# Kernel tuning notes

Measured on AMD Instinct MI355X. Metric: run time of the kernel, lower is better.

The kernel has to match this reference:

```python
import jax, jax.numpy as jnp
import numpy as np

B = 1048576
VEC_SZ = 4
LUT_BITS = 8
K = 2 ** LUT_BITS  # 256 codewords


def setup_inputs() -> dict:
    key = jax.random.key(0)
    kx, kt = jax.random.split(key)
    X = jax.random.normal(kx, (B, VEC_SZ), dtype=jnp.float32)
    tlut = jax.random.normal(kt, (K, VEC_SZ), dtype=jnp.float32)  # codebook [K, vec_sz]
    return {"X": X, "tlut": tlut}


def reference(X, tlut):
    # torch.cdist(X, tlut) -> argmin is equivalent to argmin of squared distances:
    x_sq = jnp.sum(X * X, axis=-1, keepdims=True)            # [B, 1]
    c_sq = jnp.sum(tlut * tlut, axis=-1)                     # [K]
    cross = jnp.einsum('bd,kd->bk', X, tlut)                 # [B, K]
    dist2 = x_sq - 2.0 * cross + c_sq                        # [B, K]
    state = jnp.argmin(dist2, axis=-1).astype(jnp.int32)     # [B]
    hatX = jnp.take(tlut, state, axis=0)                     # gather reconstruction [B, vec_sz]
    return hatX, state
```

## Files before the change

kernel.cpp:

```cpp
#include <hip/hip_runtime.h>

#define K_CW 256
#define PPT 4

struct P8 { float4 a; float4 b; };

__global__ void vq_pack_kernel(const float* __restrict__ tlut, float* __restrict__ pk) {
    int k = threadIdx.x;
    float c0 = tlut[k * 4 + 0];
    float c1 = tlut[k * 4 + 1];
    float c2 = tlut[k * 4 + 2];
    float c3 = tlut[k * 4 + 3];
    float s = __fadd_rn(__fadd_rn(__fadd_rn(__fmul_rn(c0, c0), __fmul_rn(c1, c1)),
                                  __fmul_rn(c2, c2)),
                        __fmul_rn(c3, c3));
    pk[k * 8 + 0] = c0; pk[k * 8 + 1] = c1; pk[k * 8 + 2] = c2; pk[k * 8 + 3] = c3;
    pk[k * 8 + 4] = s;  pk[k * 8 + 5] = 0.f; pk[k * 8 + 6] = 0.f; pk[k * 8 + 7] = 0.f;
}

__global__ __launch_bounds__(256, 4) void vq_argmin_kernel(
    const float* __restrict__ X,
    const float* __restrict__ tlut,
    const float* __restrict__ pk,
    float* __restrict__ outX,
    float* __restrict__ outS,
    int B) {
    const int g = blockIdx.x * 256 + threadIdx.x;
    const int stride = B / PPT;

    const float4* __restrict__ X4 = reinterpret_cast<const float4*>(X);
    const float4* __restrict__ T4 = reinterpret_cast<const float4*>(tlut);
    const P8* __restrict__ PK = reinterpret_cast<const P8*>(pk);

    float x0[PPT], x1[PPT], x2[PPT], x3[PPT], xsq[PPT], bestd[PPT];
    int besti[PPT];

    #pragma unroll
    for (int i = 0; i < PPT; ++i) {
        const float4 xv = X4[g + i * stride];
        x0[i] = xv.x; x1[i] = xv.y; x2[i] = xv.z; x3[i] = xv.w;
        xsq[i] = __fadd_rn(__fadd_rn(__fadd_rn(__fmul_rn(xv.x, xv.x), __fmul_rn(xv.y, xv.y)),
                                     __fmul_rn(xv.z, xv.z)),
                           __fmul_rn(xv.w, xv.w));
        bestd[i] = __builtin_inff();
        besti[i] = 0;
    }

    #pragma unroll 16
    for (int k = 0; k < K_CW; ++k) {
        const P8 e = PK[k];
        const float4 c = e.a;
        const float cs = e.b.x;
        #pragma unroll
        for (int i = 0; i < PPT; ++i) {
            float cross = __fmul_rn(x0[i], c.x);
            cross = __fmaf_rn(x1[i], c.y, cross);
            cross = __fmaf_rn(x2[i], c.z, cross);
            cross = __fmaf_rn(x3[i], c.w, cross);
            float t2 = __fmaf_rn(-2.0f, cross, xsq[i]);
            float d = __fadd_rn(t2, cs);
            besti[i] = (d < bestd[i]) ? k : besti[i];
            bestd[i] = fminf(d, bestd[i]);
        }
    }

    #pragma unroll
    for (int i = 0; i < PPT; ++i) {
        const int p = g + i * stride;
        reinterpret_cast<float4*>(outX)[p] = T4[besti[i]];
        outS[p] = (float)besti[i];
    }
}

extern "C" void kernel_launch(void* const* d_in, const int* in_sizes, int n_in,
                              void* d_out, int out_size, void* d_ws, size_t ws_size,
                              hipStream_t stream) {
    const float* X    = (const float*)d_in[0];
    const float* tlut = (const float*)d_in[1];
    const int B = in_sizes[0] / 4;

    float* outX = (float*)d_out;
    float* outS = outX + (size_t)B * 4;

    float* pk = (float*)d_ws;

    vq_pack_kernel<<<1, 256, 0, stream>>>(tlut, pk);

    const int groups = B / PPT;
    const int grid = groups / 256;
    vq_argmin_kernel<<<grid, 256, 0, stream>>>(X, tlut, pk, outX, outS, B);
}
```

Measured before the change: 128.9 us.

## Use packed FP32 math over codeword pairs with interleaved codebook layout

The codebook is repacked so that each record holds two codewords' components interleaved as float2 pairs. The distance computation then uses v_pk_mul/v_pk_fma/v_pk_add inline asm with scalar-register operands, so each instruction evaluates two codewords at once. Points per thread drop from 4 to 2 and the launch bound rises to 8 blocks per CU. This cuts VALU instruction count in the cross-term math, but the argmin compare/select stays scalar. The inline asm constrains scheduling and depends on the uniform codebook loads landing in SGPRs.

```diff
diff --git a/kernel.cpp b/kernel.cpp
--- a/kernel.cpp
+++ b/kernel.cpp
@@ -1,9 +1,25 @@
 #include <hip/hip_runtime.h>
 
+typedef float f32x2 __attribute__((ext_vector_type(2)));
+
 #define K_CW 256
-#define PPT 4
+#define NJ (K_CW / 2)
+#define PPT 2
 
-struct P8 { float4 a; float4 b; };
+struct PK2 { f32x2 c0, c1, c2, c3, cs, pad; };
+
+__device__ __forceinline__ f32x2 pk_mul_vs(f32x2 a, f32x2 b) {
+    f32x2 d; asm("v_pk_mul_f32 %0, %1, %2" : "=v"(d) : "v"(a), "s"(b)); return d;
+}
+__device__ __forceinline__ f32x2 pk_fma_vsv(f32x2 a, f32x2 b, f32x2 c) {
+    f32x2 d; asm("v_pk_fma_f32 %0, %1, %2, %3" : "=v"(d) : "v"(a), "s"(b), "v"(c)); return d;
+}
+__device__ __forceinline__ f32x2 pk_fma_vvv(f32x2 a, f32x2 b, f32x2 c) {
+    f32x2 d; asm("v_pk_fma_f32 %0, %1, %2, %3" : "=v"(d) : "v"(a), "v"(b), "v"(c)); return d;
+}
+__device__ __forceinline__ f32x2 pk_add_vs(f32x2 a, f32x2 b) {
+    f32x2 d; asm("v_pk_add_f32 %0, %1, %2" : "=v"(d) : "v"(a), "s"(b)); return d;
+}
 
 __global__ void vq_pack_kernel(const float* __restrict__ tlut, float* __restrict__ pk) {
     int k = threadIdx.x;
@@ -14,11 +30,13 @@
     float s = __fadd_rn(__fadd_rn(__fadd_rn(__fmul_rn(c0, c0), __fmul_rn(c1, c1)),
                                   __fmul_rn(c2, c2)),
                         __fmul_rn(c3, c3));
-    pk[k * 8 + 0] = c0; pk[k * 8 + 1] = c1; pk[k * 8 + 2] = c2; pk[k * 8 + 3] = c3;
-    pk[k * 8 + 4] = s;  pk[k * 8 + 5] = 0.f; pk[k * 8 + 6] = 0.f; pk[k * 8 + 7] = 0.f;
+    const int j = k >> 1, o = k & 1;
+    float* e = pk + j * 12;
+    e[0 + o] = c0; e[2 + o] = c1; e[4 + o] = c2; e[6 + o] = c3; e[8 + o] = s;
+    if (o == 0) { e[10] = 0.f; e[11] = 0.f; }
 }
 
-__global__ __launch_bounds__(256, 4) void vq_argmin_kernel(
+__global__ __launch_bounds__(256, 8) void vq_argmin_kernel(
     const float* __restrict__ X,
     const float* __restrict__ tlut,
     const float* __restrict__ pk,
@@ -30,37 +48,45 @@
 
     const float4* __restrict__ X4 = reinterpret_cast<const float4*>(X);
     const float4* __restrict__ T4 = reinterpret_cast<const float4*>(tlut);
-    const P8* __restrict__ PK = reinterpret_cast<const P8*>(pk);
+    const PK2* __restrict__ PKB = reinterpret_cast<const PK2*>(pk);
 
-    float x0[PPT], x1[PPT], x2[PPT], x3[PPT], xsq[PPT], bestd[PPT];
+    f32x2 xb0[PPT], xb1[PPT], xb2[PPT], xb3[PPT], xsqb[PPT];
+    float bestd[PPT];
     int besti[PPT];
 
     #pragma unroll
     for (int i = 0; i < PPT; ++i) {
         const float4 xv = X4[g + i * stride];
-        x0[i] = xv.x; x1[i] = xv.y; x2[i] = xv.z; x3[i] = xv.w;
-        xsq[i] = __fadd_rn(__fadd_rn(__fadd_rn(__fmul_rn(xv.x, xv.x), __fmul_rn(xv.y, xv.y)),
-                                     __fmul_rn(xv.z, xv.z)),
-                           __fmul_rn(xv.w, xv.w));
+        const float xsq =
+            __fadd_rn(__fadd_rn(__fadd_rn(__fmul_rn(xv.x, xv.x), __fmul_rn(xv.y, xv.y)),
+                                __fmul_rn(xv.z, xv.z)),
+                      __fmul_rn(xv.w, xv.w));
+        xb0[i] = f32x2{xv.x, xv.x};
+        xb1[i] = f32x2{xv.y, xv.y};
+        xb2[i] = f32x2{xv.z, xv.z};
+        xb3[i] = f32x2{xv.w, xv.w};
+        xsqb[i] = f32x2{xsq, xsq};
         bestd[i] = __builtin_inff();
         besti[i] = 0;
     }
+    const f32x2 m2 = f32x2{-2.0f, -2.0f};
 
     #pragma unroll 16
-    for (int k = 0; k < K_CW; ++k) {
-        const P8 e = PK[k];
-        const float4 c = e.a;
-        const float cs = e.b.x;
+    for (int j = 0; j < NJ; ++j) {
+        const PK2 e = PKB[j];
+        const int k0 = j * 2;
         #pragma unroll
         for (int i = 0; i < PPT; ++i) {
-            float cross = __fmul_rn(x0[i], c.x);
-            cross = __fmaf_rn(x1[i], c.y, cross);
-            cross = __fmaf_rn(x2[i], c.z, cross);
-            cross = __fmaf_rn(x3[i], c.w, cross);
-            float t2 = __fmaf_rn(-2.0f, cross, xsq[i]);
-            float d = __fadd_rn(t2, cs);
-            besti[i] = (d < bestd[i]) ? k : besti[i];
-            bestd[i] = fminf(d, bestd[i]);
+            f32x2 cr = pk_mul_vs(xb0[i], e.c0);
+            cr = pk_fma_vsv(xb1[i], e.c1, cr);
+            cr = pk_fma_vsv(xb2[i], e.c2, cr);
+            cr = pk_fma_vsv(xb3[i], e.c3, cr);
+            const f32x2 t2 = pk_fma_vvv(m2, cr, xsqb[i]);
+            const f32x2 d = pk_add_vs(t2, e.cs);
+            besti[i] = (d[0] < bestd[i]) ? k0 : besti[i];
+            bestd[i] = fminf(d[0], bestd[i]);
+            besti[i] = (d[1] < bestd[i]) ? (k0 + 1) : besti[i];
+            bestd[i] = fminf(d[1], bestd[i]);
         }
     }
 
```

Measured after the change: 140.7 us. +9.1%, slower.
